# Optimization experiments

Hardware: AMD Instinct MI355X
Metric: run time of the kernel (lower is better)

Reference implementation:

```python
import jax, jax.numpy as jnp
import numpy as np

VOCAB = 65
N_EMBED = 384
BLOCK = 256
N_HEAD = 6
HEAD_SIZE = 4  # forward uses sa_heads = MultiHeadAttention(4), NOT the Block stack
B, T = 128, 256


def setup_inputs() -> dict:
    key = jax.random.key(0)
    ks = jax.random.split(key, 16)
    s = lambda *sh: 0.02
    inp = {
        "idx": jax.random.randint(ks[0], (B, T), 0, VOCAB),
        "targets": jax.random.randint(ks[1], (B, T), 0, VOCAB),
        "tok_emb": jax.random.normal(ks[2], (VOCAB, N_EMBED), jnp.float32) * 0.02,
        "pos_emb": jax.random.normal(ks[3], (BLOCK, N_EMBED), jnp.float32) * 0.02,
        "Wq": jax.random.normal(ks[4], (N_HEAD, N_EMBED, HEAD_SIZE), jnp.float32) * 0.05,
        "Wk": jax.random.normal(ks[5], (N_HEAD, N_EMBED, HEAD_SIZE), jnp.float32) * 0.05,
        "Wv": jax.random.normal(ks[6], (N_HEAD, N_EMBED, HEAD_SIZE), jnp.float32) * 0.05,
        "Wproj": jax.random.normal(ks[7], (N_HEAD * HEAD_SIZE, N_EMBED), jnp.float32) * 0.05,
        "bproj": jnp.zeros((N_EMBED,), jnp.float32),
        "W1": jax.random.normal(ks[8], (N_EMBED, 4 * N_EMBED), jnp.float32) * 0.02,
        "b1": jnp.zeros((4 * N_EMBED,), jnp.float32),
        "W2": jax.random.normal(ks[9], (4 * N_EMBED, N_EMBED), jnp.float32) * 0.02,
        "b2": jnp.zeros((N_EMBED,), jnp.float32),
        "Wlm": jax.random.normal(ks[10], (N_EMBED, VOCAB), jnp.float32) * 0.02,
        "blm": jnp.zeros((VOCAB,), jnp.float32),
    }
    return inp


def _forward(idx, targets, tok_emb, pos_emb, Wq, Wk, Wv, Wproj, bproj, W1, b1, W2, b2, Wlm, blm):
    Bb, Tt = idx.shape
    x = tok_emb[idx] + pos_emb[:Tt]  # [B,T,C]
    # multi-head attention (manual, causal). NOTE: source scales by n_embed**-0.5 (C of input), not head_size.
    q = jnp.einsum("btc,hcd->bhtd", x, Wq)
    k = jnp.einsum("btc,hcd->bhtd", x, Wk)
    v = jnp.einsum("btc,hcd->bhtd", x, Wv)
    scores = jnp.einsum("bhtd,bhsd->bhts", q, k) * (N_EMBED ** -0.5)
    causal = jnp.tril(jnp.ones((Tt, Tt), bool))
    scores = jnp.where(causal, scores, -jnp.inf)
    w = jax.nn.softmax(scores, axis=-1)  # dropout = identity in eval
    attn = jnp.einsum("bhts,bhsd->bhtd", w, v)
    attn = attn.transpose(0, 2, 1, 3).reshape(Bb, Tt, N_HEAD * HEAD_SIZE)
    x = attn @ Wproj + bproj
    # feed-forward
    x = jax.nn.relu(x @ W1 + b1) @ W2 + b2
    logits = x @ Wlm + blm  # [B,T,V]
    logits_flat = logits.reshape(Bb * Tt, VOCAB)
    t_flat = targets.reshape(Bb * Tt)
    logp = jax.nn.log_softmax(logits_flat, axis=-1)
    loss = -jnp.mean(jnp.take_along_axis(logp, t_flat[:, None], axis=1))
    return logits_flat, loss


def reference(idx, targets, tok_emb, pos_emb, Wq, Wk, Wv, Wproj, bproj, W1, b1, W2, b2, Wlm, blm):
    return _forward(idx, targets, tok_emb, pos_emb, Wq, Wk, Wv, Wproj, bproj, W1, b1, W2, b2, Wlm, blm)
```

## Files before the change

kernel.cpp:

```cpp
#include <hip/hip_runtime.h>
#include <hip/hip_bf16.h>
#include <math.h>

typedef __hip_bfloat16 bf16;
typedef __attribute__((ext_vector_type(8))) short bf16x8;
typedef __attribute__((ext_vector_type(4))) float f32x4;
typedef __attribute__((ext_vector_type(8))) int i32x8;
typedef __attribute__((ext_vector_type(4))) int i32x4;
typedef unsigned char u8;
typedef unsigned int u32;

#define T_SEQ   256
#define C_EMB   384
#define NH      6
#define HS      4
#define NB      128
#define NTOK    (NB * T_SEQ)
#define VOC     65
#define FFDIM   1536
#define QKVW    72
#define PROJK   32
#define XROWS   (VOC * T_SEQ)

#define X2_SCALE    128.0f
#define W1_SCALE    128.0f
#define FF1_DESCALE (1.0f / (128.0f * 128.0f))
#define H1_SCALE    512.0f
#define W2_SCALE    128.0f
#define FF2_DESCALE (1.0f / (512.0f * 128.0f))

__device__ __forceinline__ float bf2f(bf16 x) { return __bfloat162float(x); }
__device__ __forceinline__ bf16  f2b(float x) { return __float2bfloat16(x); }
__device__ __forceinline__ short f2s(float x) { bf16 b = __float2bfloat16(x); return *reinterpret_cast<short*>(&b); }
__device__ __forceinline__ u8 f2fp8(float x) {
    return (u8)(__builtin_amdgcn_cvt_pk_fp8_f32(x, x, 0, false) & 0xff);
}
__device__ __forceinline__ u32 pk4fp8(const float* w) {
    int p = __builtin_amdgcn_cvt_pk_fp8_f32(w[0], w[1], 0, false);
    p = __builtin_amdgcn_cvt_pk_fp8_f32(w[2], w[3], p, true);
    return (u32)p;
}

__device__ __forceinline__ void glds16(const void* g, void* l) {
    __builtin_amdgcn_global_load_lds((const __attribute__((address_space(1))) void*)g,
                                     (__attribute__((address_space(3))) void*)l, 16, 0, 0);
}

__global__ void pack_all_kernel(const float* __restrict__ Wq, const float* __restrict__ Wk,
                                const float* __restrict__ Wv, const float* __restrict__ Wlm,
                                const float* __restrict__ Wproj,
                                const float* __restrict__ W1, const float* __restrict__ W2,
                                const float* __restrict__ tok_emb, const float* __restrict__ pos_emb,
                                bf16* __restrict__ WqkvT, bf16* __restrict__ WlmT,
                                bf16* __restrict__ WprojT, u8* __restrict__ W1P,
                                u8* __restrict__ W2f8, bf16* __restrict__ xtab,
                                float* __restrict__ lossbuf) {
    int blk = blockIdx.x;
    int t = threadIdx.x;
    if (blk == 0 && t == 0) { lossbuf[0] = 0.f; ((int*)lossbuf)[1] = 0; }
    if (blk < 128) {
        int n = blk;
        for (int c = t; c < C_EMB; c += 256) {
            float v = 0.f;
            if (n < QKVW) {
                int sel = n / 24, r = n % 24, h = r >> 2, d = r & 3;
                const float* W = (sel == 0) ? Wq : (sel == 1) ? Wk : Wv;
                v = W[(h * C_EMB + c) * HS + d];
            }
            WqkvT[(size_t)n * C_EMB + c] = f2b(v);
        }
    } else if (blk < 256) {
        int n = blk - 128;
        for (int c = t; c < C_EMB; c += 256)
            WlmT[(size_t)n * C_EMB + c] = f2b(n < VOC ? Wlm[(size_t)c * VOC + n] : 0.f);
    } else if (blk < 640) {
        int n = blk - 256;
        int k = t;
        if (k < PROJK)
            WprojT[(size_t)n * PROJK + k] = f2b(k < 24 ? Wproj[(size_t)k * C_EMB + n] : 0.f);
    } else if (blk < 640 + 288) {
        int fb = blk - 640;
        int n16 = fb / 3, kk = fb % 3;
        int b0 = t * 8;
        int l = b0 >> 5;
        int j0 = b0 & 31;
        int n = n16 * 16 + (l & 15);
        int kb = kk * 128 + (l >> 4) * 32 + j0;
        union { u8 b[8]; uint2 u; } pk;
        #pragma unroll
        for (int e = 0; e < 8; ++e)
            pk.b[e] = f2fp8(W1[(size_t)(kb + e) * FFDIM + n] * W1_SCALE);
        *(uint2*)&W1P[(size_t)fb * 2048 + b0] = pk.u;
    } else if (blk < 640 + 288 + 384) {
        int n = blk - 928;
        for (int k = t; k < FFDIM; k += 256)
            W2f8[(size_t)n * FFDIM + k] = f2fp8(W2[(size_t)k * C_EMB + n] * W2_SCALE);
    } else {
        int base = (blk - 1312) * 4;
        for (int r = 0; r < 4; ++r) {
            int row = base + r;
            int id = row >> 8, tt = row & 255;
            const float* te = tok_emb + (size_t)id * C_EMB;
            const float* pe = pos_emb + (size_t)tt * C_EMB;
            bf16* dst = xtab + (size_t)row * C_EMB;
            for (int c = t; c < C_EMB; c += 256)
                dst[c] = f2b(te[c] + pe[c]);
        }
    }
}

__global__ __launch_bounds__(512)
void qkv_gather_kernel(const int* __restrict__ idx, const bf16* __restrict__ xtab,
                       const bf16* __restrict__ Bt, float* __restrict__ outf) {
    __shared__ __align__(16) u8 As[16384];
    __shared__ __align__(16) u8 Bs[16384];
    __shared__ int rowid[128];
    int tid = threadIdx.x, lane = tid & 63, wave = tid >> 6;
    int bm = blockIdx.x * 128;
    int wm = (wave & 1) * 64, wn = (wave >> 1) * 32;
    int lrow = lane & 15, kq = lane >> 4;
    if (tid < 128) { int token = bm + tid; rowid[tid] = idx[token] * T_SEQ + (token & (T_SEQ - 1)); }
    __syncthreads();

    int r0 = tid >> 3;
    int s0 = (((tid & 7) * 16) - (r0 & 7) * 16) & 127;
    int c1 = tid + 512;
    int r1 = c1 >> 3;
    int s1 = (((c1 & 7) * 16) - (r1 & 7) * 16) & 127;
    const u8* xb = (const u8*)xtab;
    const u8* bb = (const u8*)Bt;
    long gA0 = (long)rowid[r0] * 768 + s0;
    long gA1 = (long)rowid[r1] * 768 + s1;
    long gB0 = (long)r0 * 768 + s0;
    long gB1 = (long)r1 * 768 + s1;
    int ro = (lrow & 7) * 16;

    f32x4 acc[4][2] = {};
    for (int k0 = 0; k0 < 768; k0 += 128) {
        glds16(xb + gA0 + k0, As + (size_t)tid * 16);
        glds16(xb + gA1 + k0, As + (size_t)c1 * 16);
        glds16(bb + gB0 + k0, Bs + (size_t)tid * 16);
        glds16(bb + gB1 + k0, Bs + (size_t)c1 * 16);
        __syncthreads();
        #pragma unroll
        for (int ks = 0; ks < 2; ++ks) {
            int off = (ks * 64 + kq * 16 + ro) & 127;
            bf16x8 af[4], bff[2];
            #pragma unroll
            for (int i = 0; i < 4; ++i)
                af[i] = *(const bf16x8*)&As[(size_t)(wm + i * 16 + lrow) * 128 + off];
            #pragma unroll
            for (int i = 0; i < 2; ++i)
                bff[i] = *(const bf16x8*)&Bs[(size_t)(wn + i * 16 + lrow) * 128 + off];
            #pragma unroll
            for (int mi = 0; mi < 4; ++mi)
                #pragma unroll
                for (int ni = 0; ni < 2; ++ni)
                    acc[mi][ni] = __builtin_amdgcn_mfma_f32_16x16x32_bf16(af[mi], bff[ni], acc[mi][ni], 0, 0, 0);
        }
        __syncthreads();
    }

    #pragma unroll
    for (int ni = 0; ni < 2; ++ni) {
        int col = wn + ni * 16 + lrow;
        if (col >= QKVW) continue;
        #pragma unroll
        for (int mi = 0; mi < 4; ++mi) {
            int orow = bm + wm + mi * 16 + kq * 4;
            #pragma unroll
            for (int r = 0; r < 4; ++r)
                outf[(size_t)(orow + r) * QKVW + col] = acc[mi][ni][r];
        }
    }
}

__global__ void attn_kernel(const float* __restrict__ qkv,
                            bf16* __restrict__ attnT) {
    int bh = blockIdx.x;
    int b = bh / NH, h = bh % NH;
    int t = threadIdx.x;
    __shared__ float4 kv[T_SEQ][2];
    const float* base = qkv + (size_t)(b * T_SEQ) * QKVW;
    kv[t][0] = *(const float4*)(base + t * QKVW + 24 + h * HS);
    kv[t][1] = *(const float4*)(base + t * QKVW + 48 + h * HS);
    __syncthreads();
    const float scale = 0.05103103630798288f;
    float4 q = *(const float4*)(base + t * QKVW + h * HS);
    float qx = q.x * scale, qy = q.y * scale, qz = q.z * scale, qw = q.w * scale;
    float sum0 = 0.f, sum1 = 0.f;
    float o0x = 0.f, o0y = 0.f, o0z = 0.f, o0w = 0.f;
    float o1x = 0.f, o1y = 0.f, o1z = 0.f, o1w = 0.f;
    int s = 0;
    for (; s + 1 <= t; s += 2) {
        float4 k0 = kv[s][0],     v0 = kv[s][1];
        float4 k1 = kv[s + 1][0], v1 = kv[s + 1][1];
        float p0 = __expf(qx * k0.x + qy * k0.y + qz * k0.z + qw * k0.w);
        float p1 = __expf(qx * k1.x + qy * k1.y + qz * k1.z + qw * k1.w);
        sum0 += p0; sum1 += p1;
        o0x += p0 * v0.x; o0y += p0 * v0.y; o0z += p0 * v0.z; o0w += p0 * v0.w;
        o1x += p1 * v1.x; o1y += p1 * v1.y; o1z += p1 * v1.z; o1w += p1 * v1.w;
    }
    if (s <= t) {
        float4 k0 = kv[s][0], v0 = kv[s][1];
        float p0 = __expf(qx * k0.x + qy * k0.y + qz * k0.z + qw * k0.w);
        sum0 += p0;
        o0x += p0 * v0.x; o0y += p0 * v0.y; o0z += p0 * v0.z; o0w += p0 * v0.w;
    }
    float inv = 1.f / (sum0 + sum1);
    bf16* out = attnT + (size_t)(b * T_SEQ + t) * PROJK + h * HS;
    out[0] = f2b((o0x + o1x) * inv);
    out[1] = f2b((o0y + o1y) * inv);
    out[2] = f2b((o0z + o1z) * inv);
    out[3] = f2b((o0w + o1w) * inv);
    if (h == 0) {
        bf16* pad = attnT + (size_t)(b * T_SEQ + t) * PROJK + 24;
        *(uint4*)pad = uint4{0, 0, 0, 0};
    }
}

__global__ __launch_bounds__(512, 2)
void ff1_kernel(const bf16* __restrict__ attnT, const bf16* __restrict__ WprojT,
                const float* __restrict__ bproj,
                const u8* __restrict__ W1P, const float* __restrict__ b1,
                u8* __restrict__ h1f8) {
    __shared__ __align__(16) u8 smem[81920];
    u8* x2_lds = smem;
    u8* h1s    = smem + 49152;
    short* As_p = (short*)(smem + 49152);
    short* Bs_p = (short*)(smem + 57344);

    int tid  = threadIdx.x;
    int lane = tid & 63;
    int wave = tid >> 6;
    int bm   = blockIdx.x * 128;
    int lrow  = lane & 15;
    int khalf = lane >> 4;

    {
        int row = tid >> 2;
        int i0 = (tid & 3) * 16;
        int selem = ((i0 - ((row >> 1) & 3) * 16) & 63) >> 1;
        glds16(attnT + (size_t)(bm + row) * PROJK + selem, As_p + (size_t)tid * 8);
        #pragma unroll
        for (int p = 0; p < 3; ++p) {
            int c = tid + p * 512;
            int rowb = c >> 2;
            int sel2 = (((c & 3) * 16 - ((rowb >> 1) & 3) * 16) & 63) >> 1;
            glds16(WprojT + (size_t)rowb * PROJK + sel2, Bs_p + (size_t)c * 8);
        }
    }
    __syncthreads();

    {
        int wmP = (wave & 1) * 64;
        int wn6 = (wave >> 1) * 96;
        int arot16 = ((lrow >> 1) & 3) * 16;
        int roff = ((khalf * 16 + arot16) & 63) >> 1;
        #pragma unroll
        for (int ph = 0; ph < 2; ++ph) {
            f32x4 accp[4][3] = {};
            bf16x8 afp[4], bfp[3];
            #pragma unroll
            for (int i = 0; i < 4; ++i)
                afp[i] = *(const bf16x8*)&As_p[(size_t)(wmP + i * 16 + lrow) * 32 + roff];
            #pragma unroll
            for (int i = 0; i < 3; ++i)
                bfp[i] = *(const bf16x8*)&Bs_p[(size_t)(wn6 + (ph * 3 + i) * 16 + lrow) * 32 + roff];
            #pragma unroll
            for (int mi = 0; mi < 4; ++mi)
                #pragma unroll
                for (int ni = 0; ni < 3; ++ni)
                    accp[mi][ni] = __builtin_amdgcn_mfma_f32_16x16x32_bf16(bfp[ni], afp[mi], accp[mi][ni], 0, 0, 0);
            #pragma unroll
            for (int mi = 0; mi < 4; ++mi) {
                int m = wmP + mi * 16 + lrow;
                #pragma unroll
                for (int ni = 0; ni < 3; ++ni) {
                    int n0 = wn6 + (ph * 3 + ni) * 16 + khalf * 4;
                    float4 bv = *(const float4*)(bproj + n0);
                    float w[4];
                    w[0] = (accp[mi][ni][0] + bv.x) * X2_SCALE;
                    w[1] = (accp[mi][ni][1] + bv.y) * X2_SCALE;
                    w[2] = (accp[mi][ni][2] + bv.z) * X2_SCALE;
                    w[3] = (accp[mi][ni][3] + bv.w) * X2_SCALE;
                    *(u32*)&x2_lds[(size_t)(n0 >> 7) * 16384 + (size_t)m * 128 +
                                   (((n0 & 127) + (m & 7) * 16) & 127)] = pk4fp8(w);
                }
            }
        }
    }
    __syncthreads();

    int wm1 = (wave & 3) * 32;
    int wc  = wave >> 2;
    int arot8 = (lrow & 7) * 16;
    int off0 = (khalf * 32 + arot8) & 127;
    int off1 = (off0 + 16) & 127;

    for (int nt = 0; nt < 6; ++nt) {
        f32x4 acc1[2][8] = {};
        #pragma unroll
        for (int kk = 0; kk < 3; ++kk) {
            const u8* abase = x2_lds + (size_t)kk * 16384;
            i32x8 a[2];
            #pragma unroll
            for (int i = 0; i < 2; ++i) {
                const u8* rp = abase + (size_t)(wm1 + i * 16 + lrow) * 128;
                i32x4 lo = *(const i32x4*)(rp + off0);
                i32x4 hi = *(const i32x4*)(rp + off1);
                a[i][0]=lo[0]; a[i][1]=lo[1]; a[i][2]=lo[2]; a[i][3]=lo[3];
                a[i][4]=hi[0]; a[i][5]=hi[1]; a[i][6]=hi[2]; a[i][7]=hi[3];
            }
            const u8* wbase = W1P + ((size_t)((nt * 16 + wc * 8) * 3 + kk)) * 2048
                                  + (size_t)lane * 32;
            #pragma unroll
            for (int j = 0; j < 8; ++j) {
                const u8* p = wbase + (size_t)j * 3 * 2048;
                i32x4 lo = *(const i32x4*)p;
                i32x4 hi = *(const i32x4*)(p + 16);
                i32x8 b;
                b[0]=lo[0]; b[1]=lo[1]; b[2]=lo[2]; b[3]=lo[3];
                b[4]=hi[0]; b[5]=hi[1]; b[6]=hi[2]; b[7]=hi[3];
                #pragma unroll
                for (int mi = 0; mi < 2; ++mi)
                    acc1[mi][j] = __builtin_amdgcn_mfma_scale_f32_16x16x128_f8f6f4(
                        b, a[mi], acc1[mi][j], 0, 0,
                        0, 0x7f7f7f7f, 0, 0x7f7f7f7f);
            }
        }

        #pragma unroll
        for (int mi = 0; mi < 2; ++mi) {
            int m = wm1 + mi * 16 + lrow;
            #pragma unroll
            for (int ni = 0; ni < 8; ++ni) {
                int n0 = wc * 128 + ni * 16 + khalf * 4;
                float4 bv = *(const float4*)(b1 + nt * 256 + n0);
                float w[4];
                w[0] = fmaxf(acc1[mi][ni][0] * FF1_DESCALE + bv.x, 0.f) * H1_SCALE;
                w[1] = fmaxf(acc1[mi][ni][1] * FF1_DESCALE + bv.y, 0.f) * H1_SCALE;
                w[2] = fmaxf(acc1[mi][ni][2] * FF1_DESCALE + bv.z, 0.f) * H1_SCALE;
                w[3] = fmaxf(acc1[mi][ni][3] * FF1_DESCALE + bv.w, 0.f) * H1_SCALE;
                *(u32*)&h1s[(size_t)m * 256 + ((n0 + (m & 7) * 16) & 255)] = pk4fp8(w);
            }
        }
        __syncthreads();

        #pragma unroll
        for (int p = 0; p < 4; ++p) {
            int c = tid + p * 512;
            int row = c >> 4;
            int g0 = (c & 15) * 16;
            uint4 v = *(const uint4*)&h1s[(size_t)row * 256 + ((g0 + (row & 7) * 16) & 255)];
            *(uint4*)&h1f8[(size_t)(bm + row) * FFDIM + nt * 256 + g0] = v;
        }
        __syncthreads();
    }
}

__global__ __launch_bounds__(512)
void gemm_fp8_kernel(const u8* __restrict__ A, const u8* __restrict__ Bt,
                     const float* __restrict__ bias,
                     bf16* __restrict__ outb, u8* __restrict__ outf8,
                     float descale, float oscale,
                     int M, int K, int Nout, int NT, int relu) {
    __shared__ u8 smem[32768];
    u8* As = smem;
    u8* Bs = smem + 16384;
    int lin  = blockIdx.x;
    int xcd  = lin & 7;
    int loc  = lin >> 3;
    int nt   = loc % NT;
    int mloc = loc / NT;
    int MPX  = (M / 128) >> 3;
    int bm = (xcd * MPX + mloc) * 128;
    int bn = nt * 128;

    int tid  = threadIdx.x;
    int lane = tid & 63;
    int wave = tid >> 6;
    int wm = (wave & 1) * 64;
    int wn = (wave >> 1) * 32;
    int lrow  = lane & 15;
    int khalf = lane >> 4;

    f32x4 acc[4][2] = {};
    int r0 = tid >> 3;
    int i0 = (tid & 7) * 16;
    int s0 = (i0 - (r0 & 7) * 16) & 127;
    int arot = (lrow & 7) * 16;
    int off0 = (khalf * 32 + arot) & 127;
    int off1 = (off0 + 16) & 127;

    for (int k0 = 0; k0 < K; k0 += 128) {
        const u8* Ag = A  + (size_t)(bm + r0) * K + k0 + s0;
        const u8* Bg = Bt + (size_t)(bn + r0) * K + k0 + s0;
        glds16(Ag,                  As + (size_t)tid * 16);
        glds16(Ag + (size_t)64 * K, As + 8192 + (size_t)tid * 16);
        glds16(Bg,                  Bs + (size_t)tid * 16);
        glds16(Bg + (size_t)64 * K, Bs + 8192 + (size_t)tid * 16);
        __syncthreads();

        i32x8 a[4], b[2];
        #pragma unroll
        for (int i = 0; i < 4; ++i) {
            const u8* rp = As + (size_t)(wm + i * 16 + lrow) * 128;
            i32x4 lo = *(const i32x4*)(rp + off0);
            i32x4 hi = *(const i32x4*)(rp + off1);
            a[i][0]=lo[0]; a[i][1]=lo[1]; a[i][2]=lo[2]; a[i][3]=lo[3];
            a[i][4]=hi[0]; a[i][5]=hi[1]; a[i][6]=hi[2]; a[i][7]=hi[3];
        }
        #pragma unroll
        for (int i = 0; i < 2; ++i) {
            const u8* rp = Bs + (size_t)(wn + i * 16 + lrow) * 128;
            i32x4 lo = *(const i32x4*)(rp + off0);
            i32x4 hi = *(const i32x4*)(rp + off1);
            b[i][0]=lo[0]; b[i][1]=lo[1]; b[i][2]=lo[2]; b[i][3]=lo[3];
            b[i][4]=hi[0]; b[i][5]=hi[1]; b[i][6]=hi[2]; b[i][7]=hi[3];
        }
        #pragma unroll
        for (int mi = 0; mi < 4; ++mi)
            #pragma unroll
            for (int ni = 0; ni < 2; ++ni)
                acc[mi][ni] = __builtin_amdgcn_mfma_scale_f32_16x16x128_f8f6f4(
                    b[ni], a[mi], acc[mi][ni], 0, 0,
                    0, 0x7f7f7f7f, 0, 0x7f7f7f7f);
        __syncthreads();
    }

    if (outf8) {
        #pragma unroll
        for (int mi = 0; mi < 4; ++mi) {
            int m = wm + mi * 16 + lrow;
            #pragma unroll
            for (int ni = 0; ni < 2; ++ni) {
                int n0 = wn + ni * 16 + khalf * 4;
                float4 bv = *(const float4*)(bias + bn + n0);
                float w[4];
                w[0] = acc[mi][ni][0] * descale + bv.x;
                w[1] = acc[mi][ni][1] * descale + bv.y;
                w[2] = acc[mi][ni][2] * descale + bv.z;
                w[3] = acc[mi][ni][3] * descale + bv.w;
                if (relu) {
                    w[0] = fmaxf(w[0], 0.f); w[1] = fmaxf(w[1], 0.f);
                    w[2] = fmaxf(w[2], 0.f); w[3] = fmaxf(w[3], 0.f);
                }
                w[0] *= oscale; w[1] *= oscale; w[2] *= oscale; w[3] *= oscale;
                *(u32*)&smem[(size_t)m * 128 + ((n0 + (m & 7) * 16) & 127)] = pk4fp8(w);
            }
        }
        __syncthreads();
        #pragma unroll
        for (int p = 0; p < 2; ++p) {
            int c = tid + p * 512;
            int row = c >> 3;
            int g0 = (c & 7) * 16;
            uint4 v = *(const uint4*)&smem[(size_t)row * 128 + ((g0 + (row & 7) * 16) & 127)];
            *(uint4*)&outf8[(size_t)(bm + row) * Nout + bn + g0] = v;
        }
    } else {
        short* Es = (short*)smem;
        #pragma unroll
        for (int mi = 0; mi < 4; ++mi) {
            int m = wm + mi * 16 + lrow;
            #pragma unroll
            for (int ni = 0; ni < 2; ++ni) {
                int n0 = wn + ni * 16 + khalf * 4;
                float4 bv = *(const float4*)(bias + bn + n0);
                union { short s[4]; uint2 u; } pk;
                pk.s[0] = f2s(acc[mi][ni][0] * descale + bv.x);
                pk.s[1] = f2s(acc[mi][ni][1] * descale + bv.y);
                pk.s[2] = f2s(acc[mi][ni][2] * descale + bv.z);
                pk.s[3] = f2s(acc[mi][ni][3] * descale + bv.w);
                *(uint2*)&Es[(size_t)m * 128 + ((n0 + (m & 7) * 8) & 127)] = pk.u;
            }
        }
        __syncthreads();
        #pragma unroll
        for (int p = 0; p < 4; ++p) {
            int c = tid + p * 512;
            int row = c >> 4;
            int g0 = (c & 15) * 16;
            uint4 v = *(const uint4*)&smem[(size_t)row * 256 + ((g0 + (row & 7) * 16) & 255)];
            *(uint4*)((u8*)outb + ((size_t)(bm + row) * Nout + bn) * 2 + g0) = v;
        }
    }
}

__global__ __launch_bounds__(512)
void lm_loss_kernel(const bf16* __restrict__ A, const bf16* __restrict__ Bt,
                    const float* __restrict__ bias, const int* __restrict__ targets,
                    float* __restrict__ outf, float* __restrict__ lossbuf,
                    float* __restrict__ out_loss, int M, int K) {
    __shared__ short As[128][32];
    __shared__ short Bs[128][32];
    __shared__ float Ls[128][66];
    __shared__ float red[128];
    int tid  = threadIdx.x;
    int lane = tid & 63;
    int wave = tid >> 6;
    int bm = blockIdx.x * 128;
    int wm = (wave & 1) * 64;
    int wn = (wave >> 1) * 32;
    int lrow  = lane & 15;
    int khalf = lane >> 4;

    int row = tid >> 2;
    int i0 = (tid & 3) * 16;
    int selem = ((i0 - ((row >> 1) & 3) * 16) & 63) >> 1;
    int arot = ((lrow >> 1) & 3) * 16;
    int roff = ((khalf * 16 + arot) & 63) >> 1;

    f32x4 acc[4][2] = {};
    for (int k0 = 0; k0 < K; k0 += 32) {
        glds16(A  + (size_t)(bm + row) * K + k0 + selem, (short*)As + (size_t)tid * 8);
        glds16(Bt + (size_t)row * K + k0 + selem,        (short*)Bs + (size_t)tid * 8);
        __syncthreads();

        bf16x8 af[4], bff[2];
        #pragma unroll
        for (int i = 0; i < 4; ++i)
            af[i] = *(const bf16x8*)&As[wm + i * 16 + lrow][roff];
        #pragma unroll
        for (int i = 0; i < 2; ++i)
            bff[i] = *(const bf16x8*)&Bs[wn + i * 16 + lrow][roff];
        #pragma unroll
        for (int mi = 0; mi < 4; ++mi)
            #pragma unroll
            for (int ni = 0; ni < 2; ++ni)
                acc[mi][ni] = __builtin_amdgcn_mfma_f32_16x16x32_bf16(af[mi], bff[ni], acc[mi][ni], 0, 0, 0);
        __syncthreads();
    }

    #pragma unroll
    for (int ni = 0; ni < 2; ++ni) {
        int col = wn + ni * 16 + lrow;
        if (col >= VOC) continue;
        float bv = bias[col];
        #pragma unroll
        for (int mi = 0; mi < 4; ++mi) {
            int lr = wm + mi * 16 + khalf * 4;
            #pragma unroll
            for (int r = 0; r < 4; ++r) {
                float v = acc[mi][ni][r] + bv;
                outf[(size_t)(bm + lr + r) * VOC + col] = v;
                Ls[lr + r][col] = v;
            }
        }
    }
    __syncthreads();

    if (tid < 128) {
        int token = bm + tid;
        int tgt = targets[token];
        float m = -1e30f, s = 0.f;
        #pragma unroll 8
        for (int c = 0; c < VOC; ++c) {
            float v = Ls[tid][c];
            float mn = fmaxf(m, v);
            s = s * __expf(m - mn) + __expf(v - mn);
            m = mn;
        }
        red[tid] = m + logf(s) - Ls[tid][tgt];
    }
    __syncthreads();
    if (tid < 64) {
        float s = red[tid] + red[tid + 64];
        #pragma unroll
        for (int off = 32; off > 0; off >>= 1) s += __shfl_xor(s, off);
        if (tid == 0) {
            atomicAdd(&lossbuf[0], s);
            __threadfence();
            int done = atomicAdd(&((int*)lossbuf)[1], 1);
            if (done == (NTOK / 128) - 1) {
                __threadfence();
                float total = atomicAdd(&lossbuf[0], 0.0f);
                out_loss[0] = total / (float)NTOK;
            }
        }
    }
}

extern "C" void kernel_launch(void* const* d_in, const int* in_sizes, int n_in,
                              void* d_out, int out_size, void* d_ws, size_t ws_size,
                              hipStream_t stream) {
    const int*   idx     = (const int*)  d_in[0];
    const int*   targets = (const int*)  d_in[1];
    const float* tok_emb = (const float*)d_in[2];
    const float* pos_emb = (const float*)d_in[3];
    const float* Wq      = (const float*)d_in[4];
    const float* Wk      = (const float*)d_in[5];
    const float* Wv      = (const float*)d_in[6];
    const float* Wproj   = (const float*)d_in[7];
    const float* bproj   = (const float*)d_in[8];
    const float* W1      = (const float*)d_in[9];
    const float* b1      = (const float*)d_in[10];
    const float* W2      = (const float*)d_in[11];
    const float* b2      = (const float*)d_in[12];
    const float* Wlm     = (const float*)d_in[13];
    const float* blm     = (const float*)d_in[14];

    char* ws = (char*)d_ws;
    bf16*  WprojT = (bf16*) (ws + 0);
    float* qkvbuf = (float*)(ws + 25165824);
    bf16*  attnT  = (bf16*) (ws + 34603008);
    bf16*  xtab   = (bf16*) (ws + 37748736);
    u8*    h1f8   = (u8*)   (ws + 62914560);
    bf16*  x3     = (bf16*) (ws + 163577856);
    float* lossbuf= (float*)(ws + 188743680);
    u8*    W1P    = (u8*)   (ws + 188874752);
    u8*    W2f8   = (u8*)   (ws + 190054400);
    bf16*  WqkvT  = (bf16*) (ws + 191234048);
    bf16*  WlmT   = (bf16*) (ws + 191332352);

    float* out_logits = (float*)d_out;
    float* out_loss   = out_logits + (size_t)NTOK * VOC;

    pack_all_kernel<<<1312 + XROWS / 4, 256, 0, stream>>>(
        Wq, Wk, Wv, Wlm, Wproj, W1, W2, tok_emb, pos_emb,
        WqkvT, WlmT, WprojT, W1P, W2f8, xtab, lossbuf);

    qkv_gather_kernel<<<NTOK / 128, 512, 0, stream>>>(idx, xtab, WqkvT, qkvbuf);
    attn_kernel<<<NB * NH, T_SEQ, 0, stream>>>(qkvbuf, attnT);

    ff1_kernel<<<NTOK / 128, 512, 0, stream>>>(attnT, WprojT, bproj, W1P, b1, h1f8);

    gemm_fp8_kernel<<<(NTOK / 128) * (C_EMB / 128), 512, 0, stream>>>(h1f8, W2f8, b2,
                                                                      x3, nullptr,
                                                                      FF2_DESCALE, 1.0f,
                                                                      NTOK, FFDIM, C_EMB, C_EMB / 128, 0);

    lm_loss_kernel<<<NTOK / 128, 512, 0, stream>>>(x3, WlmT, blm, targets,
                                                   out_logits, lossbuf, out_loss, NTOK, C_EMB);
}
```

Baseline: 231.9 us.

## Shrink ff1 LDS footprint for higher occupancy and widen lm_loss K-tiles

In ff1_kernel the projection GEMM operands are now read directly from global memory instead of being staged through LDS. The h1 staging tile is halved (128-column chunks over 12 iterations), which cuts shared memory from 80KB to 64KB and raises the launch-bounds occupancy hint from 2 to 4 blocks. The lm_loss kernel now loads 128-byte (64 bf16) K-chunks per barrier instead of 32-element chunks, with a rotated swizzle, so it needs 6 sync pairs instead of 12. The risks are more ff1 loop iterations and syncs, and unstaged, less coalesced global reads for the projection operands.

```diff
diff --git a/kernel.cpp b/kernel.cpp
--- a/kernel.cpp
+++ b/kernel.cpp
@@ -219,16 +219,14 @@
     }
 }
 
-__global__ __launch_bounds__(512, 2)
+__global__ __launch_bounds__(512, 4)
 void ff1_kernel(const bf16* __restrict__ attnT, const bf16* __restrict__ WprojT,
                 const float* __restrict__ bproj,
                 const u8* __restrict__ W1P, const float* __restrict__ b1,
                 u8* __restrict__ h1f8) {
-    __shared__ __align__(16) u8 smem[81920];
+    __shared__ __align__(16) u8 smem[65536];
     u8* x2_lds = smem;
     u8* h1s    = smem + 49152;
-    short* As_p = (short*)(smem + 49152);
-    short* Bs_p = (short*)(smem + 57344);
 
     int tid  = threadIdx.x;
     int lane = tid & 63;
@@ -238,35 +236,18 @@
     int khalf = lane >> 4;
 
     {
-        int row = tid >> 2;
-        int i0 = (tid & 3) * 16;
-        int selem = ((i0 - ((row >> 1) & 3) * 16) & 63) >> 1;
-        glds16(attnT + (size_t)(bm + row) * PROJK + selem, As_p + (size_t)tid * 8);
-        #pragma unroll
-        for (int p = 0; p < 3; ++p) {
-            int c = tid + p * 512;
-            int rowb = c >> 2;
-            int sel2 = (((c & 3) * 16 - ((rowb >> 1) & 3) * 16) & 63) >> 1;
-            glds16(WprojT + (size_t)rowb * PROJK + sel2, Bs_p + (size_t)c * 8);
-        }
-    }
-    __syncthreads();
-
-    {
         int wmP = (wave & 1) * 64;
         int wn6 = (wave >> 1) * 96;
-        int arot16 = ((lrow >> 1) & 3) * 16;
-        int roff = ((khalf * 16 + arot16) & 63) >> 1;
         #pragma unroll
         for (int ph = 0; ph < 2; ++ph) {
             f32x4 accp[4][3] = {};
             bf16x8 afp[4], bfp[3];
             #pragma unroll
             for (int i = 0; i < 4; ++i)
-                afp[i] = *(const bf16x8*)&As_p[(size_t)(wmP + i * 16 + lrow) * 32 + roff];
+                afp[i] = *(const bf16x8*)&attnT[(size_t)(bm + wmP + i * 16 + lrow) * PROJK + khalf * 8];
             #pragma unroll
             for (int i = 0; i < 3; ++i)
-                bfp[i] = *(const bf16x8*)&Bs_p[(size_t)(wn6 + (ph * 3 + i) * 16 + lrow) * 32 + roff];
+                bfp[i] = *(const bf16x8*)&WprojT[(size_t)(wn6 + (ph * 3 + i) * 16 + lrow) * PROJK + khalf * 8];
             #pragma unroll
             for (int mi = 0; mi < 4; ++mi)
                 #pragma unroll
@@ -298,8 +279,8 @@
     int off0 = (khalf * 32 + arot8) & 127;
     int off1 = (off0 + 16) & 127;
 
-    for (int nt = 0; nt < 6; ++nt) {
-        f32x4 acc1[2][8] = {};
+    for (int nt = 0; nt < 12; ++nt) {
+        f32x4 acc1[2][4] = {};
         #pragma unroll
         for (int kk = 0; kk < 3; ++kk) {
             const u8* abase = x2_lds + (size_t)kk * 16384;
@@ -312,10 +293,10 @@
                 a[i][0]=lo[0]; a[i][1]=lo[1]; a[i][2]=lo[2]; a[i][3]=lo[3];
                 a[i][4]=hi[0]; a[i][5]=hi[1]; a[i][6]=hi[2]; a[i][7]=hi[3];
             }
-            const u8* wbase = W1P + ((size_t)((nt * 16 + wc * 8) * 3 + kk)) * 2048
+            const u8* wbase = W1P + ((size_t)((nt * 8 + wc * 4) * 3 + kk)) * 2048
                                   + (size_t)lane * 32;
             #pragma unroll
-            for (int j = 0; j < 8; ++j) {
+            for (int j = 0; j < 4; ++j) {
                 const u8* p = wbase + (size_t)j * 3 * 2048;
                 i32x4 lo = *(const i32x4*)p;
                 i32x4 hi = *(const i32x4*)(p + 16);
@@ -334,26 +315,26 @@
         for (int mi = 0; mi < 2; ++mi) {
             int m = wm1 + mi * 16 + lrow;
             #pragma unroll
-            for (int ni = 0; ni < 8; ++ni) {
-                int n0 = wc * 128 + ni * 16 + khalf * 4;
-                float4 bv = *(const float4*)(b1 + nt * 256 + n0);
+            for (int ni = 0; ni < 4; ++ni) {
+                int n0 = wc * 64 + ni * 16 + khalf * 4;
+                float4 bv = *(const float4*)(b1 + nt * 128 + n0);
                 float w[4];
                 w[0] = fmaxf(acc1[mi][ni][0] * FF1_DESCALE + bv.x, 0.f) * H1_SCALE;
                 w[1] = fmaxf(acc1[mi][ni][1] * FF1_DESCALE + bv.y, 0.f) * H1_SCALE;
                 w[2] = fmaxf(acc1[mi][ni][2] * FF1_DESCALE + bv.z, 0.f) * H1_SCALE;
                 w[3] = fmaxf(acc1[mi][ni][3] * FF1_DESCALE + bv.w, 0.f) * H1_SCALE;
-                *(u32*)&h1s[(size_t)m * 256 + ((n0 + (m & 7) * 16) & 255)] = pk4fp8(w);
-            }
-        }
-        __syncthreads();
-
-        #pragma unroll
-        for (int p = 0; p < 4; ++p) {
+                *(u32*)&h1s[(size_t)m * 128 + ((n0 + (m & 7) * 16) & 127)] = pk4fp8(w);
+            }
+        }
+        __syncthreads();
+
+        #pragma unroll
+        for (int p = 0; p < 2; ++p) {
             int c = tid + p * 512;
-            int row = c >> 4;
-            int g0 = (c & 15) * 16;
-            uint4 v = *(const uint4*)&h1s[(size_t)row * 256 + ((g0 + (row & 7) * 16) & 255)];
-            *(uint4*)&h1f8[(size_t)(bm + row) * FFDIM + nt * 256 + g0] = v;
+            int row = c >> 3;
+            int g0 = (c & 7) * 16;
+            uint4 v = *(const uint4*)&h1s[(size_t)row * 128 + ((g0 + (row & 7) * 16) & 127)];
+            *(uint4*)&h1f8[(size_t)(bm + row) * FFDIM + nt * 128 + g0] = v;
         }
         __syncthreads();
     }
@@ -492,9 +473,9 @@
 void lm_loss_kernel(const bf16* __restrict__ A, const bf16* __restrict__ Bt,
                     const float* __restrict__ bias, const int* __restrict__ targets,
                     float* __restrict__ outf, float* __restrict__ lossbuf,
-                    float* __restrict__ out_loss, int M, int K) {
-    __shared__ short As[128][32];
-    __shared__ short Bs[128][32];
+                    float* __restrict__ out_loss) {
+    __shared__ __align__(16) u8 As[16384];
+    __shared__ __align__(16) u8 Bs[16384];
     __shared__ float Ls[128][66];
     __shared__ float red[128];
     int tid  = threadIdx.x;
@@ -506,30 +487,42 @@
     int lrow  = lane & 15;
     int khalf = lane >> 4;
 
-    int row = tid >> 2;
-    int i0 = (tid & 3) * 16;
-    int selem = ((i0 - ((row >> 1) & 3) * 16) & 63) >> 1;
-    int arot = ((lrow >> 1) & 3) * 16;
-    int roff = ((khalf * 16 + arot) & 63) >> 1;
+    int r0 = tid >> 3;
+    int s0 = (((tid & 7) * 16) - (r0 & 7) * 16) & 127;
+    int c1 = tid + 512;
+    int r1 = c1 >> 3;
+    int s1 = (((c1 & 7) * 16) - (r1 & 7) * 16) & 127;
+    const u8* ab = (const u8*)A;
+    const u8* bb = (const u8*)Bt;
+    long gA0 = (long)(bm + r0) * 768 + s0;
+    long gA1 = (long)(bm + r1) * 768 + s1;
+    long gB0 = (long)r0 * 768 + s0;
+    long gB1 = (long)r1 * 768 + s1;
+    int ro = (lrow & 7) * 16;
 
     f32x4 acc[4][2] = {};
-    for (int k0 = 0; k0 < K; k0 += 32) {
-        glds16(A  + (size_t)(bm + row) * K + k0 + selem, (short*)As + (size_t)tid * 8);
-        glds16(Bt + (size_t)row * K + k0 + selem,        (short*)Bs + (size_t)tid * 8);
-        __syncthreads();
-
-        bf16x8 af[4], bff[2];
-        #pragma unroll
-        for (int i = 0; i < 4; ++i)
-            af[i] = *(const bf16x8*)&As[wm + i * 16 + lrow][roff];
-        #pragma unroll
-        for (int i = 0; i < 2; ++i)
-            bff[i] = *(const bf16x8*)&Bs[wn + i * 16 + lrow][roff];
-        #pragma unroll
-        for (int mi = 0; mi < 4; ++mi)
-            #pragma unroll
-            for (int ni = 0; ni < 2; ++ni)
-                acc[mi][ni] = __builtin_amdgcn_mfma_f32_16x16x32_bf16(af[mi], bff[ni], acc[mi][ni], 0, 0, 0);
+    for (int k0 = 0; k0 < 768; k0 += 128) {
+        glds16(ab + gA0 + k0, As + (size_t)tid * 16);
+        glds16(ab + gA1 + k0, As + (size_t)c1 * 16);
+        glds16(bb + gB0 + k0, Bs + (size_t)tid * 16);
+        glds16(bb + gB1 + k0, Bs + (size_t)c1 * 16);
+        __syncthreads();
+        #pragma unroll
+        for (int ks = 0; ks < 2; ++ks) {
+            int off = (ks * 64 + khalf * 16 + ro) & 127;
+            bf16x8 af[4], bff[2];
+            #pragma unroll
+            for (int i = 0; i < 4; ++i)
+                af[i] = *(const bf16x8*)&As[(size_t)(wm + i * 16 + lrow) * 128 + off];
+            #pragma unroll
+            for (int i = 0; i < 2; ++i)
+                bff[i] = *(const bf16x8*)&Bs[(size_t)(wn + i * 16 + lrow) * 128 + off];
+            #pragma unroll
+            for (int mi = 0; mi < 4; ++mi)
+                #pragma unroll
+                for (int ni = 0; ni < 2; ++ni)
+                    acc[mi][ni] = __builtin_amdgcn_mfma_f32_16x16x32_bf16(af[mi], bff[ni], acc[mi][ni], 0, 0, 0);
+        }
         __syncthreads();
     }
 
@@ -632,5 +625,5 @@
                                                                       NTOK, FFDIM, C_EMB, C_EMB / 128, 0);
 
     lm_loss_kernel<<<NTOK / 128, 512, 0, stream>>>(x3, WlmT, blm, targets,
-                                                   out_logits, lossbuf, out_loss, NTOK, C_EMB);
-}
+                                                   out_logits, lossbuf, out_loss);
+}
```

After: 239.6 us. +3.3%, slower.
